# Kernel tuning notes

Measured on AMD Instinct MI355X. Metric: run time of the kernel, lower is better.

## Reference

```python
import jax, jax.numpy as jnp
import numpy as np

NUM_CLASSES = 5  # sleep stages: W, N1, N2, N3, REM
N = 4194304


def setup_inputs() -> dict:
    key = jax.random.key(0)
    k1, k2 = jax.random.split(key)
    inputs = jax.random.normal(k1, (N, NUM_CLASSES), dtype=jnp.float32)
    targets = jax.random.randint(k2, (N,), 0, NUM_CLASSES, dtype=jnp.int32)
    return {"inputs": inputs, "targets": targets}


def reference(inputs, targets):
    # Mean False Error loss: per-class mean of per-sample cross-entropy,
    # summed over classes that are present in the batch.
    # per-sample CE loss (stable log-softmax, single pass)
    logp = jax.nn.log_softmax(inputs, axis=-1)                    # [N, C]
    per_sample = -jnp.take_along_axis(logp, targets[:, None].astype(jnp.int32), axis=1)[:, 0]  # [N]
    # segment-reduce by class label (replaces the python grouping loop)
    loss_sums = jax.ops.segment_sum(per_sample, targets, num_segments=NUM_CLASSES)             # [C]
    counts = jax.ops.segment_sum(jnp.ones_like(per_sample), targets, num_segments=NUM_CLASSES) # [C]
    # per-class mean; empty classes contribute 0
    means = jnp.where(counts > 0, loss_sums / jnp.maximum(counts, 1.0), 0.0)
    return jnp.sum(means)
```

## Files before the change

### kernel.cpp

```cpp
#include <hip/hip_runtime.h>

#define NCLS 5
#define NSAMP 4194304
#define BLOCK 256
#define GRID 1024
#define NTHREADS (GRID * BLOCK)
#define ITERS (NSAMP / (NTHREADS * 4))
#define NVALS (2 * NCLS)

__device__ __forceinline__ void accum_sample(float l0, float l1, float l2, float l3, float l4,
                                             int t, float sums[NCLS], float cnts[NCLS]) {
    float m = fmaxf(fmaxf(fmaxf(l0, l1), fmaxf(l2, l3)), l4);
    float s = __expf(l0 - m) + __expf(l1 - m) + __expf(l2 - m) +
              __expf(l3 - m) + __expf(l4 - m);
    float lt = (t == 0) ? l0 : (t == 1) ? l1 : (t == 2) ? l2 : (t == 3) ? l3 : l4;
    float ce = __logf(s) + m - lt;
#pragma unroll
    for (int k = 0; k < NCLS; ++k) {
        bool hit = (t == k);
        sums[k] += hit ? ce : 0.0f;
        cnts[k] += hit ? 1.0f : 0.0f;
    }
}

__device__ __forceinline__ void block_reduce_10(float sums[NCLS], float cnts[NCLS],
                                                float* result10 ) {
#pragma unroll
    for (int k = 0; k < NCLS; ++k) {
#pragma unroll
        for (int off = 32; off > 0; off >>= 1) {
            sums[k] += __shfl_down(sums[k], off, 64);
            cnts[k] += __shfl_down(cnts[k], off, 64);
        }
    }
    __shared__ float ls[BLOCK / 64][NVALS];
    const int lane = threadIdx.x & 63;
    const int wave = threadIdx.x >> 6;
    if (lane == 0) {
#pragma unroll
        for (int k = 0; k < NCLS; ++k) {
            ls[wave][k] = sums[k];
            ls[wave][NCLS + k] = cnts[k];
        }
    }
    __syncthreads();
    if (threadIdx.x < NVALS) {
        float v = 0.f;
#pragma unroll
        for (int w = 0; w < BLOCK / 64; ++w) v += ls[w][threadIdx.x];
        *result10 = v;
    }
}

__global__ __launch_bounds__(BLOCK) void mfe_partial(const float* __restrict__ inputs,
                                                     const int* __restrict__ targets,
                                                     float* __restrict__ partial ) {
    const int tid = blockIdx.x * BLOCK + threadIdx.x;

    float sums[NCLS] = {0.f, 0.f, 0.f, 0.f, 0.f};
    float cnts[NCLS] = {0.f, 0.f, 0.f, 0.f, 0.f};

#pragma unroll
    for (int it = 0; it < ITERS; ++it) {
        const int chunk = it * NTHREADS + tid;
        const int base = chunk * 4;
        const float4* in4 = (const float4*)(inputs + (size_t)base * NCLS);
        float4 a = in4[0];
        float4 b = in4[1];
        float4 c = in4[2];
        float4 d = in4[3];
        float4 e = in4[4];
        int4 t4 = *(const int4*)(targets + base);

        accum_sample(a.x, a.y, a.z, a.w, b.x, t4.x, sums, cnts);
        accum_sample(b.y, b.z, b.w, c.x, c.y, t4.y, sums, cnts);
        accum_sample(c.z, c.w, d.x, d.y, d.z, t4.z, sums, cnts);
        accum_sample(d.w, e.x, e.y, e.z, e.w, t4.w, sums, cnts);
    }

    float total;
    block_reduce_10(sums, cnts, &total);
    if (threadIdx.x < NVALS) {
        partial[threadIdx.x * GRID + blockIdx.x] = total;
    }
}

__global__ __launch_bounds__(BLOCK) void mfe_final(const float* __restrict__ partial,
                                                   float* __restrict__ out) {
    float sums[NCLS];
    float cnts[NCLS];
#pragma unroll
    for (int k = 0; k < NCLS; ++k) {
        float s = 0.f, c = 0.f;
#pragma unroll
        for (int i = 0; i < GRID / BLOCK; ++i) {
            s += partial[k * GRID + threadIdx.x + i * BLOCK];
            c += partial[(NCLS + k) * GRID + threadIdx.x + i * BLOCK];
        }
        sums[k] = s;
        cnts[k] = c;
    }

    float total;
    block_reduce_10(sums, cnts, &total);

    __shared__ float fin[NVALS];
    if (threadIdx.x < NVALS) fin[threadIdx.x] = total;
    __syncthreads();
    if (threadIdx.x == 0) {
        float loss = 0.f;
#pragma unroll
        for (int k = 0; k < NCLS; ++k) {
            float cnt = fin[NCLS + k];
            if (cnt > 0.f) loss += fin[k] / cnt;
        }
        out[0] = loss;
    }
}

extern "C" void kernel_launch(void* const* d_in, const int* in_sizes, int n_in,
                              void* d_out, int out_size, void* d_ws, size_t ws_size,
                              hipStream_t stream) {
    const float* inputs = (const float*)d_in[0];
    const int* targets = (const int*)d_in[1];
    float* out = (float*)d_out;
    float* partial = (float*)d_ws;

    mfe_partial<<<GRID, BLOCK, 0, stream>>>(inputs, targets, partial);
    mfe_final<<<1, BLOCK, 0, stream>>>(partial, out);
}
```

Measured before the change: 137.5 us.

## Fuse partial and final reduction via atomic counter; prefetch next iteration's loads

Merges the two-kernel reduction into one kernel where the last block to finish, detected with an atomic counter and thread fences, performs the final reduction. It also adds register double-buffering so the next iteration's input and target loads are issued before the current samples are processed. The goal is to remove the separate final-kernel launch and raise memory-level parallelism at low occupancy. It adds a memset per call, extra registers for the prefetch buffers, and atomic/fence overhead.

Result: slower. 288.6 us (+110.0%).

```diff
diff --git a/kernel.cpp b/kernel.cpp
--- a/kernel.cpp
+++ b/kernel.cpp
@@ -24,7 +24,7 @@
 }
 
 __device__ __forceinline__ void block_reduce_10(float sums[NCLS], float cnts[NCLS],
-                                                float* result10 ) {
+                                                float* result10) {
 #pragma unroll
     for (int k = 0; k < NCLS; ++k) {
 #pragma unroll
@@ -50,32 +50,44 @@
         for (int w = 0; w < BLOCK / 64; ++w) v += ls[w][threadIdx.x];
         *result10 = v;
     }
+    __syncthreads();
 }
 
-__global__ __launch_bounds__(BLOCK) void mfe_partial(const float* __restrict__ inputs,
-                                                     const int* __restrict__ targets,
-                                                     float* __restrict__ partial ) {
+__global__ __launch_bounds__(BLOCK) void mfe_fused(const float* __restrict__ inputs,
+                                                   const int* __restrict__ targets,
+                                                   float* __restrict__ partial ,
+                                                   int* __restrict__ counter,
+                                                   float* __restrict__ out) {
     const int tid = blockIdx.x * BLOCK + threadIdx.x;
 
     float sums[NCLS] = {0.f, 0.f, 0.f, 0.f, 0.f};
     float cnts[NCLS] = {0.f, 0.f, 0.f, 0.f, 0.f};
 
+    float4 a, b, c, d, e;
+    int4 t4;
+    {
+        const int base = tid * 4;
+        const float4* in4 = (const float4*)(inputs + (size_t)base * NCLS);
+        a = in4[0]; b = in4[1]; c = in4[2]; d = in4[3]; e = in4[4];
+        t4 = *(const int4*)(targets + base);
+    }
 #pragma unroll
     for (int it = 0; it < ITERS; ++it) {
-        const int chunk = it * NTHREADS + tid;
-        const int base = chunk * 4;
-        const float4* in4 = (const float4*)(inputs + (size_t)base * NCLS);
-        float4 a = in4[0];
-        float4 b = in4[1];
-        float4 c = in4[2];
-        float4 d = in4[3];
-        float4 e = in4[4];
-        int4 t4 = *(const int4*)(targets + base);
-
+        float4 an, bn, cn, dn, en;
+        int4 tn;
+        if (it + 1 < ITERS) {
+            const int base = ((it + 1) * NTHREADS + tid) * 4;
+            const float4* in4 = (const float4*)(inputs + (size_t)base * NCLS);
+            an = in4[0]; bn = in4[1]; cn = in4[2]; dn = in4[3]; en = in4[4];
+            tn = *(const int4*)(targets + base);
+        }
         accum_sample(a.x, a.y, a.z, a.w, b.x, t4.x, sums, cnts);
         accum_sample(b.y, b.z, b.w, c.x, c.y, t4.y, sums, cnts);
         accum_sample(c.z, c.w, d.x, d.y, d.z, t4.z, sums, cnts);
         accum_sample(d.w, e.x, e.y, e.z, e.w, t4.w, sums, cnts);
+        if (it + 1 < ITERS) {
+            a = an; b = bn; c = cn; d = dn; e = en; t4 = tn;
+        }
     }
 
     float total;
@@ -83,38 +95,44 @@
     if (threadIdx.x < NVALS) {
         partial[threadIdx.x * GRID + blockIdx.x] = total;
     }
-}
+    __threadfence();
 
-__global__ __launch_bounds__(BLOCK) void mfe_final(const float* __restrict__ partial,
-                                                   float* __restrict__ out) {
-    float sums[NCLS];
-    float cnts[NCLS];
-#pragma unroll
-    for (int k = 0; k < NCLS; ++k) {
-        float s = 0.f, c = 0.f;
-#pragma unroll
-        for (int i = 0; i < GRID / BLOCK; ++i) {
-            s += partial[k * GRID + threadIdx.x + i * BLOCK];
-            c += partial[(NCLS + k) * GRID + threadIdx.x + i * BLOCK];
-        }
-        sums[k] = s;
-        cnts[k] = c;
+    __shared__ int s_last;
+    if (threadIdx.x == 0) {
+        int old = atomicAdd(counter, 1);
+        s_last = (old == GRID - 1) ? 1 : 0;
     }
+    __syncthreads();
 
-    float total;
-    block_reduce_10(sums, cnts, &total);
-
-    __shared__ float fin[NVALS];
-    if (threadIdx.x < NVALS) fin[threadIdx.x] = total;
-    __syncthreads();
-    if (threadIdx.x == 0) {
-        float loss = 0.f;
+    if (s_last) {
+        __threadfence();
+        float fs[NCLS], fc[NCLS];
 #pragma unroll
         for (int k = 0; k < NCLS; ++k) {
-            float cnt = fin[NCLS + k];
-            if (cnt > 0.f) loss += fin[k] / cnt;
+            float s = 0.f, cc = 0.f;
+#pragma unroll
+            for (int i = 0; i < GRID / BLOCK; ++i) {
+                s += partial[k * GRID + threadIdx.x + i * BLOCK];
+                cc += partial[(NCLS + k) * GRID + threadIdx.x + i * BLOCK];
+            }
+            fs[k] = s;
+            fc[k] = cc;
         }
-        out[0] = loss;
+        float ftot;
+        block_reduce_10(fs, fc, &ftot);
+
+        __shared__ float fin[NVALS];
+        if (threadIdx.x < NVALS) fin[threadIdx.x] = ftot;
+        __syncthreads();
+        if (threadIdx.x == 0) {
+            float loss = 0.f;
+#pragma unroll
+            for (int k = 0; k < NCLS; ++k) {
+                float cnt = fin[NCLS + k];
+                if (cnt > 0.f) loss += fin[k] / cnt;
+            }
+            out[0] = loss;
+        }
     }
 }
 
@@ -125,7 +143,8 @@
     const int* targets = (const int*)d_in[1];
     float* out = (float*)d_out;
     float* partial = (float*)d_ws;
+    int* counter = (int*)((char*)d_ws + NVALS * GRID * sizeof(float));
 
-    mfe_partial<<<GRID, BLOCK, 0, stream>>>(inputs, targets, partial);
-    mfe_final<<<1, BLOCK, 0, stream>>>(partial, out);
+    hipMemsetAsync(counter, 0, sizeof(int), stream);
+    mfe_fused<<<GRID, BLOCK, 0, stream>>>(inputs, targets, partial, counter, out);
 }
```
